# Kernel optimization log

Hardware: AMD Instinct MI355X
Metric: run time of the kernel (lower is better)

## Reference

```python
import jax, jax.numpy as jnp
import numpy as np

EMB = 512
HEADS = 8

def setup_inputs() -> dict:
    key = jax.random.key(0)
    ks = jax.random.split(key, 9)
    s = 1.0 / np.sqrt(EMB)
    return {
        'x':  jax.random.normal(ks[0], (4, 2048, EMB), dtype=jnp.float32),
        'Wq': jax.random.uniform(ks[1], (EMB, EMB), jnp.float32, -s, s),
        'bq': jax.random.uniform(ks[2], (EMB,), jnp.float32, -s, s),
        'Wk': jax.random.uniform(ks[3], (EMB, EMB), jnp.float32, -s, s),
        'bk': jax.random.uniform(ks[4], (EMB,), jnp.float32, -s, s),
        'Wv': jax.random.uniform(ks[5], (EMB, EMB), jnp.float32, -s, s),
        'bv': jax.random.uniform(ks[6], (EMB,), jnp.float32, -s, s),
        'Wo': jax.random.uniform(ks[7], (EMB, EMB), jnp.float32, -s, s),
        'bo': jax.random.uniform(ks[8], (EMB,), jnp.float32, -s, s),
    }

def reference(x, Wq, bq, Wk, bk, Wv, bv, Wo, bo):
    b, n, e = x.shape
    h = HEADS
    d = e // h
    def split_heads(t):
        return t.reshape(b, n, h, d).transpose(0, 2, 1, 3)  # b h n d
    q = split_heads(x @ Wq.T + bq)
    k = split_heads(x @ Wk.T + bk)
    v = split_heads(x @ Wv.T + bv)
    energy = jnp.einsum('bhqd,bhkd->bhqk', q, k)
    scaling = jnp.sqrt(jnp.float32(e))  # NOTE: sqrt(emb_size), not sqrt(head_dim), per source
    att = jax.nn.softmax(energy / scaling, axis=-1)
    out = jnp.einsum('bhal,bhlv->bhav', att, v)  # b h n d
    out = out.transpose(0, 2, 1, 3).reshape(b, n, e)
    return out @ Wo.T + bo
```

## Files before the change

### kernel.cpp

```cpp
#include <hip/hip_runtime.h>

typedef float f32x4 __attribute__((ext_vector_type(4)));
typedef float f32x16 __attribute__((ext_vector_type(16)));
typedef short bf16x8 __attribute__((ext_vector_type(8)));
typedef unsigned int uint;
typedef unsigned short ushort_t;

#define EMB    512
#define NSEQ   2048
#define NBATCH 4
#define NHEAD  8
#define MROWS  (NBATCH * NSEQ)
#define CEXP   0.06375872f

__device__ __forceinline__ uint f2bf(float x) {
    uint u = __builtin_bit_cast(uint, x);
    return (u + 0x7fffu + ((u >> 16) & 1u)) >> 16;
}

__device__ __forceinline__ void glds16(const void* g, void* l) {
    __builtin_amdgcn_global_load_lds(
        (const __attribute__((address_space(1))) uint*)g,
        (__attribute__((address_space(3))) uint*)l, 16, 0, 0);
}

__global__ __launch_bounds__(256)
void prep(const float* __restrict__ x,
          const float* __restrict__ Wq, const float* __restrict__ Wk,
          const float* __restrict__ Wv, const float* __restrict__ Wo,
          const float* __restrict__ bq, const float* __restrict__ bk,
          const float* __restrict__ bv,
          ushort_t* __restrict__ xb, ushort_t* __restrict__ Wqkvb,
          float* __restrict__ bqkv, ushort_t* __restrict__ Wob) {
    int t = blockIdx.x * 256 + threadIdx.x;
    {
        float4 v = ((const float4*)x)[t];
        uint2 p;
        p.x = f2bf(v.x) | (f2bf(v.y) << 16);
        p.y = f2bf(v.z) | (f2bf(v.w) << 16);
        ((uint2*)xb)[t] = p;
    }
    if (t < 65536) {
        float4 a = ((const float4*)Wq)[t];
        float4 b = ((const float4*)Wk)[t];
        float4 c = ((const float4*)Wv)[t];
        float4 d = ((const float4*)Wo)[t];
        uint2 p;
        p.x = f2bf(a.x) | (f2bf(a.y) << 16); p.y = f2bf(a.z) | (f2bf(a.w) << 16);
        ((uint2*)Wqkvb)[t] = p;
        p.x = f2bf(b.x) | (f2bf(b.y) << 16); p.y = f2bf(b.z) | (f2bf(b.w) << 16);
        ((uint2*)Wqkvb)[t + 65536] = p;
        p.x = f2bf(c.x) | (f2bf(c.y) << 16); p.y = f2bf(c.z) | (f2bf(c.w) << 16);
        ((uint2*)Wqkvb)[t + 131072] = p;
        p.x = f2bf(d.x) | (f2bf(d.y) << 16); p.y = f2bf(d.z) | (f2bf(d.w) << 16);
        ((uint2*)Wob)[t] = p;
    }
    if (t < 512) {
        bqkv[t] = bq[t]; bqkv[512 + t] = bk[t]; bqkv[1024 + t] = bv[t];
    }
}

template<int MODE>
__global__ __launch_bounds__(256)
void gemm64(const ushort_t* __restrict__ A, const ushort_t* __restrict__ BT,
            const float* __restrict__ bias, ushort_t* __restrict__ oQK,
            ushort_t* __restrict__ oVT, float* __restrict__ oC) {
    __shared__ __align__(16) char smem[32768];
    ushort_t (*As)[2][64][32] = (ushort_t (*)[2][64][32])smem;
    ushort_t (*Bs)[2][64][32] = (ushort_t (*)[2][64][32])(smem + 16384);
    float (*ep)[68] = (float (*)[68])smem;

    const int tid = threadIdx.x, wave = tid >> 6, lane = tid & 63;
    const int m0 = blockIdx.x * 64, n0 = blockIdx.y * 64;
    const int wr = (wave & 1) * 32, wc = (wave >> 1) * 32;

    f32x4 acc[2][2];
#pragma unroll
    for (int i = 0; i < 2; ++i)
#pragma unroll
        for (int j = 0; j < 2; ++j) acc[i][j] = (f32x4){0.f, 0.f, 0.f, 0.f};

    const int grow = wave * 16 + (lane >> 2);
    const int gcol = (lane & 3) * 8;
    const ushort_t* Ag = A  + (size_t)(m0 + grow) * 512 + gcol;
    const ushort_t* Bg = BT + (size_t)(n0 + grow) * 512 + gcol;
    const int fr = lane & 15, fc = (lane >> 4) * 8;

#pragma unroll
    for (int t = 0; t < 2; ++t) {
        glds16(Ag + t * 32, &As[0][t][wave * 16][0]);
        glds16(Bg + t * 32, &Bs[0][t][wave * 16][0]);
    }
    __syncthreads();

    int p = 0;
    for (int kt = 0; kt < 8; ++kt) {
        if (kt < 7) {
#pragma unroll
            for (int t = 0; t < 2; ++t) {
                glds16(Ag + (kt + 1) * 64 + t * 32, &As[p ^ 1][t][wave * 16][0]);
                glds16(Bg + (kt + 1) * 64 + t * 32, &Bs[p ^ 1][t][wave * 16][0]);
            }
        }
#pragma unroll
        for (int t = 0; t < 2; ++t) {
            bf16x8 af[2], bf[2];
#pragma unroll
            for (int i = 0; i < 2; ++i) af[i] = *(const bf16x8*)&As[p][t][wr + i * 16 + fr][fc];
#pragma unroll
            for (int j = 0; j < 2; ++j) bf[j] = *(const bf16x8*)&Bs[p][t][wc + j * 16 + fr][fc];
#pragma unroll
            for (int i = 0; i < 2; ++i)
#pragma unroll
                for (int j = 0; j < 2; ++j)
                    acc[i][j] = __builtin_amdgcn_mfma_f32_16x16x32_bf16(af[i], bf[j], acc[i][j], 0, 0, 0);
        }
        __syncthreads();
        p ^= 1;
    }

    const int col_l = lane & 15, row_l = (lane >> 4) * 4;

    if (MODE == 0 && n0 >= 1024) {
#pragma unroll
        for (int j = 0; j < 2; ++j) {
            const int col = n0 + wc + j * 16 + col_l;
            const float bv = bias[col];
#pragma unroll
            for (int i = 0; i < 2; ++i) {
                const int row = m0 + wr + i * 16 + row_l;
                f32x4 v = acc[i][j];
                v += (f32x4){bv, bv, bv, bv};
                const int e = col - 1024;
                const int b = row >> 11, tok = row & 2047;
                uint2 p2;
                p2.x = f2bf(v[0]) | (f2bf(v[1]) << 16);
                p2.y = f2bf(v[2]) | (f2bf(v[3]) << 16);
                *(uint2*)&oVT[((size_t)(b * 512 + e)) * 2048 + tok] = p2;
            }
        }
        return;
    }

    const float scale = (MODE == 0 && n0 < 512) ? CEXP : 1.0f;
    float bv[2];
#pragma unroll
    for (int j = 0; j < 2; ++j) bv[j] = bias[n0 + wc + j * 16 + col_l];

    const int erow = tid >> 3, eseg = (tid & 7) * 8;
#pragma unroll
    for (int c = 0; c < 2; ++c) {
        __syncthreads();
        if (wr == c * 32) {
#pragma unroll
            for (int i = 0; i < 2; ++i) {
#pragma unroll
                for (int j = 0; j < 2; ++j) {
                    f32x4 v = acc[i][j];
#pragma unroll
                    for (int r = 0; r < 4; ++r)
                        ep[i * 16 + row_l + r][wc + j * 16 + col_l] = (v[r] + bv[j]) * scale;
                }
            }
        }
        __syncthreads();
        const int grow2 = m0 + c * 32 + erow;
        if (MODE == 0) {
            uint4 o0;
#pragma unroll
            for (int k = 0; k < 4; ++k) {
                ((uint*)&o0)[k] = f2bf(ep[erow][eseg + k * 2])
                                | (f2bf(ep[erow][eseg + k * 2 + 1]) << 16);
            }
            *(uint4*)&oQK[(size_t)grow2 * 1024 + n0 + eseg] = o0;
        } else {
#pragma unroll
            for (int k = 0; k < 2; ++k) {
                f32x4 v = *(const f32x4*)&ep[erow][eseg + k * 4];
                *(f32x4*)&oC[(size_t)grow2 * 512 + n0 + eseg + k * 4] = v;
            }
        }
    }
}

template<int NSLICE>
__global__ __launch_bounds__(256, 2)
void attn_mfma(const ushort_t* __restrict__ QK, const ushort_t* __restrict__ VT,
               ushort_t* __restrict__ Op, float* __restrict__ Lp,
               ushort_t* __restrict__ AO) {
    __shared__ ushort_t Ks[2][64][72];
    __shared__ ushort_t Vs[2][64][72];

    const int tid = threadIdx.x, w = tid >> 6, lane = tid & 63;
    const int qt = blockIdx.x, bh = blockIdx.y, b = bh >> 3, h = bh & 7;
    const int slice = (NSLICE > 1) ? blockIdx.z : 0;
    const int l31 = lane & 31, lhi = lane >> 5;

    const int tok0 = qt * 256 + w * 64 + l31;
    bf16x8 qf[2][4];
#pragma unroll
    for (int g = 0; g < 2; ++g)
#pragma unroll
        for (int ks = 0; ks < 4; ++ks)
            qf[g][ks] = *(const bf16x8*)&QK[(size_t)(b * NSEQ + tok0 + g * 32) * 1024
                                            + h * 64 + ks * 16 + lhi * 8];

    f32x16 accO[2][2];
    f32x16 accL[2];
#pragma unroll
    for (int g = 0; g < 2; ++g) {
#pragma unroll
        for (int i = 0; i < 16; ++i) { accO[g][0][i] = 0.f; accO[g][1][i] = 0.f; accL[g][i] = 0.f; }
    }
    union { uint u[4]; bf16x8 v; } ONE;
    ONE.u[0] = 0x3f803f80u; ONE.u[1] = 0x3f803f80u;
    ONE.u[2] = 0x3f803f80u; ONE.u[3] = 0x3f803f80u;

    const int sr = tid & 63, sc = (tid >> 6) * 16;
    const ushort_t* Kg = QK + (size_t)(b * NSEQ) * 1024 + 512 + h * 64;
    const ushort_t* Vg = VT + ((size_t)(b * 512 + h * 64)) * 2048;

    const int kt0 = slice * (32 / NSLICE), kt1 = kt0 + 32 / NSLICE;

    {
        const int k0 = kt0 * 64;
        uint4 kv0 = *(const uint4*)&Kg[(size_t)(k0 + sr) * 1024 + sc];
        uint4 kv1 = *(const uint4*)&Kg[(size_t)(k0 + sr) * 1024 + sc + 8];
        uint4 vv0 = *(const uint4*)&Vg[(size_t)sr * 2048 + k0 + sc];
        uint4 vv1 = *(const uint4*)&Vg[(size_t)sr * 2048 + k0 + sc + 8];
        *(uint4*)&Ks[0][sr][sc] = kv0;  *(uint4*)&Ks[0][sr][sc + 8] = kv1;
        *(uint4*)&Vs[0][sr][sc] = vv0;  *(uint4*)&Vs[0][sr][sc + 8] = vv1;
        __syncthreads();
    }

    const uint psel = 0x07060302u;
    int p = 0;
#pragma unroll 2
    for (int kt = kt0; kt < kt1; ++kt) {
        uint4 kv0, kv1, vv0, vv1;
        const bool pf = (kt + 1 < kt1);
        if (pf) {
            const int k0 = (kt + 1) * 64;
            kv0 = *(const uint4*)&Kg[(size_t)(k0 + sr) * 1024 + sc];
            kv1 = *(const uint4*)&Kg[(size_t)(k0 + sr) * 1024 + sc + 8];
            vv0 = *(const uint4*)&Vg[(size_t)sr * 2048 + k0 + sc];
            vv1 = *(const uint4*)&Vg[(size_t)sr * 2048 + k0 + sc + 8];
        }

#pragma unroll
        for (int ms = 0; ms < 2; ++ms) {
            bf16x8 ka[4];
#pragma unroll
            for (int ks = 0; ks < 4; ++ks)
                ka[ks] = *(const bf16x8*)&Ks[p][ms * 32 + l31][ks * 16 + lhi * 8];

            f32x16 st[2];
#pragma unroll
            for (int g = 0; g < 2; ++g)
#pragma unroll
                for (int i = 0; i < 16; ++i) st[g][i] = 0.f;
            __builtin_amdgcn_s_setprio(1);
#pragma unroll
            for (int ks = 0; ks < 4; ++ks) {
                st[0] = __builtin_amdgcn_mfma_f32_32x32x16_bf16(ka[ks], qf[0][ks], st[0], 0, 0, 0);
                st[1] = __builtin_amdgcn_mfma_f32_32x32x16_bf16(ka[ks], qf[1][ks], st[1], 0, 0, 0);
            }
            __builtin_amdgcn_s_setprio(0);

            uint dd[2][8];
#pragma unroll
            for (int g = 0; g < 2; ++g)
#pragma unroll
                for (int i = 0; i < 8; ++i) {
                    uint ua = __builtin_bit_cast(uint, __builtin_amdgcn_exp2f(st[g][2 * i]));
                    uint ub = __builtin_bit_cast(uint, __builtin_amdgcn_exp2f(st[g][2 * i + 1]));
                    uint r;
                    asm("v_perm_b32 %0, %1, %2, %3" : "=v"(r) : "v"(ub), "v"(ua), "v"(psel));
                    dd[g][i] = r;
                }

#pragma unroll
            for (int s = 0; s < 2; ++s) {
                const int step = ms * 2 + s;
                bf16x8 va0 = *(const bf16x8*)&Vs[p][l31][step * 16 + lhi * 8];
                bf16x8 va1 = *(const bf16x8*)&Vs[p][32 + l31][step * 16 + lhi * 8];
#pragma unroll
                for (int g = 0; g < 2; ++g) {
                    uint a0 = dd[g][4 * s + 0], a2 = dd[g][4 * s + 2];
                    uint a1 = dd[g][4 * s + 1], a3 = dd[g][4 * s + 3];
                    asm("v_permlane32_swap_b32 %0, %1" : "+v"(a0), "+v"(a2));
                    asm("v_permlane32_swap_b32 %0, %1" : "+v"(a1), "+v"(a3));
                    union { uint u[4]; bf16x8 v; } B;
                    B.u[0] = a0; B.u[1] = a1; B.u[2] = a2; B.u[3] = a3;
                    __builtin_amdgcn_s_setprio(1);
                    accO[g][0] = __builtin_amdgcn_mfma_f32_32x32x16_bf16(va0, B.v, accO[g][0], 0, 0, 0);
                    accO[g][1] = __builtin_amdgcn_mfma_f32_32x32x16_bf16(va1, B.v, accO[g][1], 0, 0, 0);
                    accL[g]    = __builtin_amdgcn_mfma_f32_32x32x16_bf16(ONE.v, B.v, accL[g], 0, 0, 0);
                    __builtin_amdgcn_s_setprio(0);
                }
            }
        }

        if (pf) {
            *(uint4*)&Ks[p ^ 1][sr][sc] = kv0;  *(uint4*)&Ks[p ^ 1][sr][sc + 8] = kv1;
            *(uint4*)&Vs[p ^ 1][sr][sc] = vv0;  *(uint4*)&Vs[p ^ 1][sr][sc + 8] = vv1;
        }
        __syncthreads();
        p ^= 1;
    }

    if (NSLICE == 1) {
#pragma unroll
        for (int g = 0; g < 2; ++g) {
            const float inv = 1.0f / accL[g][0];
#pragma unroll
            for (int hf = 0; hf < 2; ++hf)
#pragma unroll
                for (int r = 0; r < 16; ++r) {
                    const int d = (r & 3) + 8 * (r >> 2) + 4 * lhi + 32 * hf;
                    AO[((size_t)(b * NSEQ + tok0 + g * 32)) * 512 + h * 64 + d] =
                        (ushort_t)f2bf(accO[g][hf][r] * inv);
                }
        }
    } else {
        if (lane < 32) {
#pragma unroll
            for (int g = 0; g < 2; ++g)
                Lp[(size_t)slice * 65536 + bh * 2048 + tok0 + g * 32] = accL[g][0];
        }
        ushort_t* Os = Op + (size_t)slice * 4194304;
#pragma unroll
        for (int g = 0; g < 2; ++g)
#pragma unroll
            for (int hf = 0; hf < 2; ++hf)
#pragma unroll
                for (int r = 0; r < 16; ++r) {
                    const int d = (r & 3) + 8 * (r >> 2) + 4 * lhi + 32 * hf;
                    Os[((size_t)(bh * 64 + d)) * 2048 + tok0 + g * 32] =
                        (ushort_t)f2bf(accO[g][hf][r]);
                }
    }
}

__global__ __launch_bounds__(256)
void combine2Tb(const ushort_t* __restrict__ Op, const float* __restrict__ Lp,
                ushort_t* __restrict__ AO) {
    __shared__ float T[64][68];
    const int tid = threadIdx.x;
    const int tc = blockIdx.x, bh = blockIdx.y;
    const int b = bh >> 3, h = bh & 7;
    const int tok0 = tc * 64;

    const int d = tid >> 2, ts = (tid & 3) * 16;
    float acc[16];
#pragma unroll
    for (int i = 0; i < 16; ++i) acc[i] = 0.f;
#pragma unroll
    for (int s = 0; s < 2; ++s) {
        const ushort_t* P = Op + (size_t)s * 4194304
                               + ((size_t)(bh * 64 + d)) * 2048 + tok0 + ts;
#pragma unroll
        for (int k2 = 0; k2 < 2; ++k2) {
            uint4 u = *(const uint4*)(P + 8 * k2);
#pragma unroll
            for (int j = 0; j < 4; ++j) {
                uint uw = ((const uint*)&u)[j];
                acc[k2 * 8 + 2 * j]     += __builtin_bit_cast(float, uw << 16);
                acc[k2 * 8 + 2 * j + 1] += __builtin_bit_cast(float, uw & 0xffff0000u);
            }
        }
    }
#pragma unroll
    for (int k = 0; k < 4; ++k)
        *(f32x4*)&T[d][ts + 4 * k] = *(const f32x4*)&acc[4 * k];
    __syncthreads();

    const int tk = tid >> 2, ds = (tid & 3) * 16;
    const int tok = tok0 + tk;
    const float inv = 1.0f / (Lp[bh * 2048 + tok] + Lp[65536 + bh * 2048 + tok]);
    uint o[8];
#pragma unroll
    for (int k = 0; k < 8; ++k) {
        float a = T[ds + 2 * k][tk] * inv;
        float c = T[ds + 2 * k + 1][tk] * inv;
        o[k] = f2bf(a) | (f2bf(c) << 16);
    }
    ushort_t* dst = AO + ((size_t)(b * NSEQ + tok)) * 512 + h * 64 + ds;
    *(uint4*)dst       = *(const uint4*)&o[0];
    *(uint4*)(dst + 8) = *(const uint4*)&o[4];
}

extern "C" void kernel_launch(void* const* d_in, const int* in_sizes, int n_in,
                              void* d_out, int out_size, void* d_ws, size_t ws_size,
                              hipStream_t stream) {
    const float* x  = (const float*)d_in[0];
    const float* Wq = (const float*)d_in[1];
    const float* bq = (const float*)d_in[2];
    const float* Wk = (const float*)d_in[3];
    const float* bk = (const float*)d_in[4];
    const float* Wv = (const float*)d_in[5];
    const float* bv = (const float*)d_in[6];
    const float* Wo = (const float*)d_in[7];
    const float* bo = (const float*)d_in[8];

    char* ws = (char*)d_ws;
    ushort_t* xb    = (ushort_t*)(ws);
    ushort_t* Wqkvb = (ushort_t*)(ws + 8388608);
    ushort_t* Wob   = (ushort_t*)(ws + 9961472);
    float*    bqkv  = (float*)   (ws + 10485760);
    ushort_t* QKb   = (ushort_t*)(ws + 10491904);
    ushort_t* VTg   = (ushort_t*)(ws + 27269120);
    ushort_t* AOb   = (ushort_t*)(ws + 35657728);
    ushort_t* Opart = (ushort_t*)(ws + 44046336);
    float*    Lpart = (float*)   (ws);
    const bool split = ws_size >= 78125056;

    prep<<<4096, 256, 0, stream>>>(x, Wq, Wk, Wv, Wo, bq, bk, bv,
                                   xb, Wqkvb, bqkv, Wob);
    gemm64<0><<<dim3(128, 24), 256, 0, stream>>>(xb, Wqkvb, bqkv, QKb, VTg, nullptr);
    if (split) {
        attn_mfma<2><<<dim3(8, 32, 2), 256, 0, stream>>>(QKb, VTg, Opart, Lpart, nullptr);
        combine2Tb<<<dim3(32, 32), 256, 0, stream>>>(Opart, Lpart, AOb);
    } else {
        attn_mfma<1><<<dim3(8, 32, 1), 256, 0, stream>>>(QKb, VTg, nullptr, nullptr, AOb);
    }
    gemm64<1><<<dim3(128, 8), 256, 0, stream>>>(AOb, Wob, bo, nullptr, nullptr, (float*)d_out);
}
```

Measured before the change: 167.8 us.

## Fuse split-attention combine into output projection GEMM and coalesce V-transpose stores

The separate combine2Tb kernel, which merged the two attention slices and wrote a bf16 attention-output buffer, is removed. A new gemmOut kernel reads both partial outputs and the softmax denominators directly, normalises them into its A tile in shared memory, and multiplies by Wo. This drops one launch and the round trip of the intermediate buffer, at the cost of each output-column block redoing the combine work and issuing strided scalar 16-bit global loads. Separately, the V-transpose epilogue of the QKV GEMM now stages through shared memory so each thread writes 32 contiguous bytes instead of scattered 8-byte stores.

```diff
diff --git a/kernel.cpp b/kernel.cpp
--- a/kernel.cpp
+++ b/kernel.cpp
@@ -69,6 +69,7 @@
     ushort_t (*As)[2][64][32] = (ushort_t (*)[2][64][32])smem;
     ushort_t (*Bs)[2][64][32] = (ushort_t (*)[2][64][32])(smem + 16384);
     float (*ep)[68] = (float (*)[68])smem;
+    float (*epV)[69] = (float (*)[69])smem;
 
     const int tid = threadIdx.x, wave = tid >> 6, lane = tid & 63;
     const int m0 = blockIdx.x * 64, n0 = blockIdx.y * 64;
@@ -122,23 +123,28 @@
     const int col_l = lane & 15, row_l = (lane >> 4) * 4;
 
     if (MODE == 0 && n0 >= 1024) {
+        const int e0 = n0 - 1024;
 #pragma unroll
         for (int j = 0; j < 2; ++j) {
-            const int col = n0 + wc + j * 16 + col_l;
-            const float bv = bias[col];
+            const float bvv = bias[n0 + wc + j * 16 + col_l];
 #pragma unroll
             for (int i = 0; i < 2; ++i) {
-                const int row = m0 + wr + i * 16 + row_l;
                 f32x4 v = acc[i][j];
-                v += (f32x4){bv, bv, bv, bv};
-                const int e = col - 1024;
-                const int b = row >> 11, tok = row & 2047;
-                uint2 p2;
-                p2.x = f2bf(v[0]) | (f2bf(v[1]) << 16);
-                p2.y = f2bf(v[2]) | (f2bf(v[3]) << 16);
-                *(uint2*)&oVT[((size_t)(b * 512 + e)) * 2048 + tok] = p2;
-            }
-        }
+#pragma unroll
+                for (int r = 0; r < 4; ++r)
+                    epV[wc + j * 16 + col_l][wr + i * 16 + row_l + r] = v[r] + bvv;
+            }
+        }
+        __syncthreads();
+        const int e = tid >> 2, ts = (tid & 3) * 16;
+        const int bb = m0 >> 11, tok = (m0 & 2047) + ts;
+        uint o[8];
+#pragma unroll
+        for (int k = 0; k < 8; ++k)
+            o[k] = f2bf(epV[e][ts + 2 * k]) | (f2bf(epV[e][ts + 2 * k + 1]) << 16);
+        ushort_t* dst = &oVT[((size_t)(bb * 512 + e0 + e)) * 2048 + tok];
+        *(uint4*)dst       = *(const uint4*)&o[0];
+        *(uint4*)(dst + 8) = *(const uint4*)&o[4];
         return;
     }
 
@@ -179,6 +185,116 @@
                 f32x4 v = *(const f32x4*)&ep[erow][eseg + k * 4];
                 *(f32x4*)&oC[(size_t)grow2 * 512 + n0 + eseg + k * 4] = v;
             }
+        }
+    }
+}
+
+__global__ __launch_bounds__(256)
+void gemmOut(const ushort_t* __restrict__ Op, const float* __restrict__ Lp,
+             const ushort_t* __restrict__ W, const float* __restrict__ bias,
+             float* __restrict__ oC) {
+    __shared__ __align__(16) char smem[16896];
+    ushort_t (*Ls)[68]     = (ushort_t (*)[68])smem;
+    ushort_t (*Bs)[64][32] = (ushort_t (*)[64][32])(smem + 8704);
+    float (*ep)[68]        = (float (*)[68])smem;
+
+    const int tid = threadIdx.x, wave = tid >> 6, lane = tid & 63;
+    const int m0 = blockIdx.x * 64, n0 = blockIdx.y * 64;
+    const int wr = (wave & 1) * 32, wc = (wave >> 1) * 32;
+
+    f32x4 acc[2][2];
+#pragma unroll
+    for (int i = 0; i < 2; ++i)
+#pragma unroll
+        for (int j = 0; j < 2; ++j) acc[i][j] = (f32x4){0.f, 0.f, 0.f, 0.f};
+
+    const int bb = m0 >> 11;
+    const int tok = (m0 & 2047) + lane;
+    const ushort_t* OpA = Op + ((size_t)(bb * 512)) * 2048 + tok;
+    const ushort_t* OpB = OpA + 4194304;
+    const float*    LpA = Lp + (size_t)bb * 16384 + (m0 & 2047) + lane;
+
+    const int grow = wave * 16 + (lane >> 2);
+    const int gcol = (lane & 3) * 8;
+    const ushort_t* Bg = W + (size_t)(n0 + grow) * 512 + gcol;
+    const int fr = lane & 15, fc = (lane >> 4) * 8;
+
+    uint u0[16], u1[16];
+    float l0 = LpA[0], l1 = LpA[65536];
+#pragma unroll
+    for (int eo = 0; eo < 16; ++eo) {
+        const size_t off = (size_t)(wave * 16 + eo) * 2048;
+        u0[eo] = OpA[off];  u1[eo] = OpB[off];
+    }
+
+    for (int kt = 0; kt < 8; ++kt) {
+        const float inv = 1.0f / (l0 + l1);
+        uint pk[8];
+#pragma unroll
+        for (int k = 0; k < 8; ++k) {
+            const float sa = __builtin_bit_cast(float, u0[2 * k] << 16)
+                           + __builtin_bit_cast(float, u1[2 * k] << 16);
+            const float sb = __builtin_bit_cast(float, u0[2 * k + 1] << 16)
+                           + __builtin_bit_cast(float, u1[2 * k + 1] << 16);
+            pk[k] = f2bf(sa * inv) | (f2bf(sb * inv) << 16);
+        }
+        __syncthreads();
+        *(uint4*)&Ls[lane][wave * 16]     = *(const uint4*)&pk[0];
+        *(uint4*)&Ls[lane][wave * 16 + 8] = *(const uint4*)&pk[4];
+#pragma unroll
+        for (int t = 0; t < 2; ++t)
+            glds16(Bg + kt * 64 + t * 32, &Bs[t][wave * 16][0]);
+        __syncthreads();
+
+        if (kt < 7) {
+            l0 = LpA[(kt + 1) * 2048];  l1 = LpA[65536 + (kt + 1) * 2048];
+#pragma unroll
+            for (int eo = 0; eo < 16; ++eo) {
+                const size_t off = (size_t)((kt + 1) * 64 + wave * 16 + eo) * 2048;
+                u0[eo] = OpA[off];  u1[eo] = OpB[off];
+            }
+        }
+#pragma unroll
+        for (int t = 0; t < 2; ++t) {
+            bf16x8 af[2], bf[2];
+#pragma unroll
+            for (int i = 0; i < 2; ++i) af[i] = *(const bf16x8*)&Ls[wr + i * 16 + fr][t * 32 + fc];
+#pragma unroll
+            for (int j = 0; j < 2; ++j) bf[j] = *(const bf16x8*)&Bs[t][wc + j * 16 + fr][fc];
+#pragma unroll
+            for (int i = 0; i < 2; ++i)
+#pragma unroll
+                for (int j = 0; j < 2; ++j)
+                    acc[i][j] = __builtin_amdgcn_mfma_f32_16x16x32_bf16(af[i], bf[j], acc[i][j], 0, 0, 0);
+        }
+    }
+
+    const int col_l = lane & 15, row_l = (lane >> 4) * 4;
+    float bv[2];
+#pragma unroll
+    for (int j = 0; j < 2; ++j) bv[j] = bias[n0 + wc + j * 16 + col_l];
+
+    const int erow = tid >> 3, eseg = (tid & 7) * 8;
+#pragma unroll
+    for (int c = 0; c < 2; ++c) {
+        __syncthreads();
+        if (wr == c * 32) {
+#pragma unroll
+            for (int i = 0; i < 2; ++i)
+#pragma unroll
+                for (int j = 0; j < 2; ++j) {
+                    f32x4 v = acc[i][j];
+#pragma unroll
+                    for (int r = 0; r < 4; ++r)
+                        ep[i * 16 + row_l + r][wc + j * 16 + col_l] = v[r] + bv[j];
+                }
+        }
+        __syncthreads();
+        const int grow2 = m0 + c * 32 + erow;
+#pragma unroll
+        for (int k = 0; k < 2; ++k) {
+            f32x4 v = *(const f32x4*)&ep[erow][eseg + k * 4];
+            *(f32x4*)&oC[(size_t)grow2 * 512 + n0 + eseg + k * 4] = v;
         }
     }
 }
@@ -420,9 +536,9 @@
     gemm64<0><<<dim3(128, 24), 256, 0, stream>>>(xb, Wqkvb, bqkv, QKb, VTg, nullptr);
     if (split) {
         attn_mfma<2><<<dim3(8, 32, 2), 256, 0, stream>>>(QKb, VTg, Opart, Lpart, nullptr);
-        combine2Tb<<<dim3(32, 32), 256, 0, stream>>>(Opart, Lpart, AOb);
+        gemmOut<<<dim3(128, 8), 256, 0, stream>>>(Opart, Lpart, Wob, bo, (float*)d_out);
     } else {
         attn_mfma<1><<<dim3(8, 32, 1), 256, 0, stream>>>(QKb, VTg, nullptr, nullptr, AOb);
-    }
-    gemm64<1><<<dim3(128, 8), 256, 0, stream>>>(AOb, Wob, bo, nullptr, nullptr, (float*)d_out);
-}
+        gemm64<1><<<dim3(128, 8), 256, 0, stream>>>(AOb, Wob, bo, nullptr, nullptr, (float*)d_out);
+    }
+}
```

New measurement: 178.4 us. +6.3%, slower.

## Stage V-transpose epilogue through LDS and double attention key tile to 128

Applied to the files above, without the earlier changes.

The QKV GEMM epilogue for the V part now writes the biased accumulators transposed into shared memory and then emits coalesced 32-byte bf16 rows into VT, replacing scattered 8-byte stores. The attention kernel now processes 128 keys per iteration instead of 64, which halves the number of barrier and prefetch rounds per block. In exchange the attention kernel uses about twice the LDS (~71KB vs ~37KB) and more prefetch registers, which may lower occupancy below the two blocks per CU requested in launch bounds.

```diff
diff --git a/kernel.cpp b/kernel.cpp
--- a/kernel.cpp
+++ b/kernel.cpp
@@ -69,6 +69,7 @@
     ushort_t (*As)[2][64][32] = (ushort_t (*)[2][64][32])smem;
     ushort_t (*Bs)[2][64][32] = (ushort_t (*)[2][64][32])(smem + 16384);
     float (*ep)[68] = (float (*)[68])smem;
+    float (*epV)[69] = (float (*)[69])smem;
 
     const int tid = threadIdx.x, wave = tid >> 6, lane = tid & 63;
     const int m0 = blockIdx.x * 64, n0 = blockIdx.y * 64;
@@ -122,23 +123,28 @@
     const int col_l = lane & 15, row_l = (lane >> 4) * 4;
 
     if (MODE == 0 && n0 >= 1024) {
+        const int e0 = n0 - 1024;
 #pragma unroll
         for (int j = 0; j < 2; ++j) {
-            const int col = n0 + wc + j * 16 + col_l;
-            const float bv = bias[col];
+            const float bvv = bias[n0 + wc + j * 16 + col_l];
 #pragma unroll
             for (int i = 0; i < 2; ++i) {
-                const int row = m0 + wr + i * 16 + row_l;
                 f32x4 v = acc[i][j];
-                v += (f32x4){bv, bv, bv, bv};
-                const int e = col - 1024;
-                const int b = row >> 11, tok = row & 2047;
-                uint2 p2;
-                p2.x = f2bf(v[0]) | (f2bf(v[1]) << 16);
-                p2.y = f2bf(v[2]) | (f2bf(v[3]) << 16);
-                *(uint2*)&oVT[((size_t)(b * 512 + e)) * 2048 + tok] = p2;
-            }
-        }
+#pragma unroll
+                for (int r = 0; r < 4; ++r)
+                    epV[wc + j * 16 + col_l][wr + i * 16 + row_l + r] = v[r] + bvv;
+            }
+        }
+        __syncthreads();
+        const int e = tid >> 2, ts = (tid & 3) * 16;
+        const int bb = m0 >> 11, tok = (m0 & 2047) + ts;
+        uint o[8];
+#pragma unroll
+        for (int k = 0; k < 8; ++k)
+            o[k] = f2bf(epV[e][ts + 2 * k]) | (f2bf(epV[e][ts + 2 * k + 1]) << 16);
+        ushort_t* dst = &oVT[((size_t)(bb * 512 + e0 + e)) * 2048 + tok];
+        *(uint4*)dst       = *(const uint4*)&o[0];
+        *(uint4*)(dst + 8) = *(const uint4*)&o[4];
         return;
     }
 
@@ -188,8 +194,8 @@
 void attn_mfma(const ushort_t* __restrict__ QK, const ushort_t* __restrict__ VT,
                ushort_t* __restrict__ Op, float* __restrict__ Lp,
                ushort_t* __restrict__ AO) {
-    __shared__ ushort_t Ks[2][64][72];
-    __shared__ ushort_t Vs[2][64][72];
+    __shared__ ushort_t Ks[2][128][72];
+    __shared__ ushort_t Vs[2][64][136];
 
     const int tid = threadIdx.x, w = tid >> 6, lane = tid & 63;
     const int qt = blockIdx.x, bh = blockIdx.y, b = bh >> 3, h = bh & 7;
@@ -220,16 +226,22 @@
     const ushort_t* Kg = QK + (size_t)(b * NSEQ) * 1024 + 512 + h * 64;
     const ushort_t* Vg = VT + ((size_t)(b * 512 + h * 64)) * 2048;
 
-    const int kt0 = slice * (32 / NSLICE), kt1 = kt0 + 32 / NSLICE;
+    const int kt0 = slice * (16 / NSLICE), kt1 = kt0 + 16 / NSLICE;
 
     {
-        const int k0 = kt0 * 64;
+        const int k0 = kt0 * 128;
         uint4 kv0 = *(const uint4*)&Kg[(size_t)(k0 + sr) * 1024 + sc];
         uint4 kv1 = *(const uint4*)&Kg[(size_t)(k0 + sr) * 1024 + sc + 8];
+        uint4 kv2 = *(const uint4*)&Kg[(size_t)(k0 + 64 + sr) * 1024 + sc];
+        uint4 kv3 = *(const uint4*)&Kg[(size_t)(k0 + 64 + sr) * 1024 + sc + 8];
         uint4 vv0 = *(const uint4*)&Vg[(size_t)sr * 2048 + k0 + sc];
         uint4 vv1 = *(const uint4*)&Vg[(size_t)sr * 2048 + k0 + sc + 8];
-        *(uint4*)&Ks[0][sr][sc] = kv0;  *(uint4*)&Ks[0][sr][sc + 8] = kv1;
-        *(uint4*)&Vs[0][sr][sc] = vv0;  *(uint4*)&Vs[0][sr][sc + 8] = vv1;
+        uint4 vv2 = *(const uint4*)&Vg[(size_t)sr * 2048 + k0 + 64 + sc];
+        uint4 vv3 = *(const uint4*)&Vg[(size_t)sr * 2048 + k0 + 64 + sc + 8];
+        *(uint4*)&Ks[0][sr][sc] = kv0;       *(uint4*)&Ks[0][sr][sc + 8] = kv1;
+        *(uint4*)&Ks[0][64 + sr][sc] = kv2;  *(uint4*)&Ks[0][64 + sr][sc + 8] = kv3;
+        *(uint4*)&Vs[0][sr][sc] = vv0;       *(uint4*)&Vs[0][sr][sc + 8] = vv1;
+        *(uint4*)&Vs[0][sr][64 + sc] = vv2;  *(uint4*)&Vs[0][sr][64 + sc + 8] = vv3;
         __syncthreads();
     }
 
@@ -237,18 +249,22 @@
     int p = 0;
 #pragma unroll 2
     for (int kt = kt0; kt < kt1; ++kt) {
-        uint4 kv0, kv1, vv0, vv1;
+        uint4 kv0, kv1, kv2, kv3, vv0, vv1, vv2, vv3;
         const bool pf = (kt + 1 < kt1);
         if (pf) {
-            const int k0 = (kt + 1) * 64;
+            const int k0 = (kt + 1) * 128;
             kv0 = *(const uint4*)&Kg[(size_t)(k0 + sr) * 1024 + sc];
             kv1 = *(const uint4*)&Kg[(size_t)(k0 + sr) * 1024 + sc + 8];
+            kv2 = *(const uint4*)&Kg[(size_t)(k0 + 64 + sr) * 1024 + sc];
+            kv3 = *(const uint4*)&Kg[(size_t)(k0 + 64 + sr) * 1024 + sc + 8];
             vv0 = *(const uint4*)&Vg[(size_t)sr * 2048 + k0 + sc];
             vv1 = *(const uint4*)&Vg[(size_t)sr * 2048 + k0 + sc + 8];
-        }
-
-#pragma unroll
-        for (int ms = 0; ms < 2; ++ms) {
+            vv2 = *(const uint4*)&Vg[(size_t)sr * 2048 + k0 + 64 + sc];
+            vv3 = *(const uint4*)&Vg[(size_t)sr * 2048 + k0 + 64 + sc + 8];
+        }
+
+#pragma unroll
+        for (int ms = 0; ms < 4; ++ms) {
             bf16x8 ka[4];
 #pragma unroll
             for (int ks = 0; ks < 4; ++ks)
@@ -302,8 +318,10 @@
         }
 
         if (pf) {
-            *(uint4*)&Ks[p ^ 1][sr][sc] = kv0;  *(uint4*)&Ks[p ^ 1][sr][sc + 8] = kv1;
-            *(uint4*)&Vs[p ^ 1][sr][sc] = vv0;  *(uint4*)&Vs[p ^ 1][sr][sc + 8] = vv1;
+            *(uint4*)&Ks[p ^ 1][sr][sc] = kv0;       *(uint4*)&Ks[p ^ 1][sr][sc + 8] = kv1;
+            *(uint4*)&Ks[p ^ 1][64 + sr][sc] = kv2;  *(uint4*)&Ks[p ^ 1][64 + sr][sc + 8] = kv3;
+            *(uint4*)&Vs[p ^ 1][sr][sc] = vv0;       *(uint4*)&Vs[p ^ 1][sr][sc + 8] = vv1;
+            *(uint4*)&Vs[p ^ 1][sr][64 + sc] = vv2;  *(uint4*)&Vs[p ^ 1][sr][64 + sc + 8] = vv3;
         }
         __syncthreads();
         p ^= 1;
```

New measurement: 167.5 us. No clear change (-0.2%).

## Stage V-transpose epilogue through LDS and remap attention blocks for XCD locality

Applied to the files above, without the earlier changes.

The V-projection epilogue now writes the biased tile transposed into shared memory and then emits coalesced 32-byte row stores into the transposed V buffer, replacing the earlier scattered 8-byte strided stores. Separately, the split attention kernel uses a flat 1-D grid with a block-index remap so that consecutive block IDs, which are distributed round-robin across XCDs, group the same (batch, head, slice) onto one XCD, aiming to improve L2 reuse of K/V. The changes add an extra barrier and an LDS pass in the epilogue, and they depend on the hardware dispatch order matching the assumed pattern.

```diff
diff --git a/kernel.cpp b/kernel.cpp
--- a/kernel.cpp
+++ b/kernel.cpp
@@ -69,6 +69,7 @@
     ushort_t (*As)[2][64][32] = (ushort_t (*)[2][64][32])smem;
     ushort_t (*Bs)[2][64][32] = (ushort_t (*)[2][64][32])(smem + 16384);
     float (*ep)[68] = (float (*)[68])smem;
+    float (*epV)[69] = (float (*)[69])smem;
 
     const int tid = threadIdx.x, wave = tid >> 6, lane = tid & 63;
     const int m0 = blockIdx.x * 64, n0 = blockIdx.y * 64;
@@ -122,23 +123,28 @@
     const int col_l = lane & 15, row_l = (lane >> 4) * 4;
 
     if (MODE == 0 && n0 >= 1024) {
+        const int e0 = n0 - 1024;
 #pragma unroll
         for (int j = 0; j < 2; ++j) {
-            const int col = n0 + wc + j * 16 + col_l;
-            const float bv = bias[col];
+            const float bvv = bias[n0 + wc + j * 16 + col_l];
 #pragma unroll
             for (int i = 0; i < 2; ++i) {
-                const int row = m0 + wr + i * 16 + row_l;
                 f32x4 v = acc[i][j];
-                v += (f32x4){bv, bv, bv, bv};
-                const int e = col - 1024;
-                const int b = row >> 11, tok = row & 2047;
-                uint2 p2;
-                p2.x = f2bf(v[0]) | (f2bf(v[1]) << 16);
-                p2.y = f2bf(v[2]) | (f2bf(v[3]) << 16);
-                *(uint2*)&oVT[((size_t)(b * 512 + e)) * 2048 + tok] = p2;
-            }
-        }
+#pragma unroll
+                for (int r = 0; r < 4; ++r)
+                    epV[wc + j * 16 + col_l][wr + i * 16 + row_l + r] = v[r] + bvv;
+            }
+        }
+        __syncthreads();
+        const int e = tid >> 2, ts = (tid & 3) * 16;
+        const int bb = m0 >> 11, tok = (m0 & 2047) + ts;
+        uint o[8];
+#pragma unroll
+        for (int k = 0; k < 8; ++k)
+            o[k] = f2bf(epV[e][ts + 2 * k]) | (f2bf(epV[e][ts + 2 * k + 1]) << 16);
+        ushort_t* dst = &oVT[((size_t)(bb * 512 + e0 + e)) * 2048 + tok];
+        *(uint4*)dst       = *(const uint4*)&o[0];
+        *(uint4*)(dst + 8) = *(const uint4*)&o[4];
         return;
     }
 
@@ -192,8 +198,17 @@
     __shared__ ushort_t Vs[2][64][72];
 
     const int tid = threadIdx.x, w = tid >> 6, lane = tid & 63;
-    const int qt = blockIdx.x, bh = blockIdx.y, b = bh >> 3, h = bh & 7;
-    const int slice = (NSLICE > 1) ? blockIdx.z : 0;
+    int qt, bh, slice;
+    if (NSLICE == 2) {
+        const int wgid = blockIdx.x;
+        const int g = (wgid & 7) | ((wgid >> 6) << 3);
+        qt = (wgid >> 3) & 7;
+        bh = g & 31;
+        slice = g >> 5;
+    } else {
+        qt = blockIdx.x; bh = blockIdx.y; slice = 0;
+    }
+    const int b = bh >> 3, h = bh & 7;
     const int l31 = lane & 31, lhi = lane >> 5;
 
     const int tok0 = qt * 256 + w * 64 + l31;
@@ -419,10 +434,10 @@
                                    xb, Wqkvb, bqkv, Wob);
     gemm64<0><<<dim3(128, 24), 256, 0, stream>>>(xb, Wqkvb, bqkv, QKb, VTg, nullptr);
     if (split) {
-        attn_mfma<2><<<dim3(8, 32, 2), 256, 0, stream>>>(QKb, VTg, Opart, Lpart, nullptr);
+        attn_mfma<2><<<dim3(512), 256, 0, stream>>>(QKb, VTg, Opart, Lpart, nullptr);
         combine2Tb<<<dim3(32, 32), 256, 0, stream>>>(Opart, Lpart, AOb);
     } else {
-        attn_mfma<1><<<dim3(8, 32, 1), 256, 0, stream>>>(QKb, VTg, nullptr, nullptr, AOb);
+        attn_mfma<1><<<dim3(8, 32), 256, 0, stream>>>(QKb, VTg, nullptr, nullptr, AOb);
     }
     gemm64<1><<<dim3(128, 8), 256, 0, stream>>>(AOb, Wob, bo, nullptr, nullptr, (float*)d_out);
 }
```

Measured after the change: 164.9 us (median of 2 runs). About the same (-1.7%).
